# Kernel tuning notes

Measured on AMD Instinct MI355X. Metric: run time of the kernel, lower is better.

Reference implementation:

```python
import jax, jax.numpy as jnp
import numpy as np

N_TP = 4  # number of heterogeneous agent types (experts)


def _mlp(x, w1, b1, w2, b2, w3, b3):
    h = jax.nn.relu(x @ w1 + b1)
    h = jax.nn.relu(h @ w2 + b2)
    return h @ w3 + b3


def setup_inputs() -> dict:
    key = jax.random.key(0)
    ks = jax.random.split(key, 12)
    T, A, D, H, NA = 2048, 128, 64, 64, 16
    s = 0.05
    return {
        "obs": jax.random.normal(ks[0], (T, A, D), dtype=jnp.float32),
        "hete_pick": jax.random.randint(ks[1], (T, A), 0, N_TP, dtype=jnp.int64),
        "gp_sel_summary": jax.random.uniform(ks[2], (T, N_TP), dtype=jnp.float32),
        "W1": jax.random.normal(ks[3], (N_TP, D + N_TP, H), dtype=jnp.float32) * s,
        "b1": jnp.zeros((N_TP, H), jnp.float32),
        "W2": jax.random.normal(ks[4], (N_TP, H, H), dtype=jnp.float32) * s,
        "b2": jnp.zeros((N_TP, H), jnp.float32),
        "W3": jax.random.normal(ks[5], (N_TP, H, NA), dtype=jnp.float32) * s,
        "b3": jnp.zeros((N_TP, NA), jnp.float32),
        "cW1": jax.random.normal(ks[6], (D + N_TP, H), dtype=jnp.float32) * s,
        "cb1": jnp.zeros((H,), jnp.float32),
        "cW2": jax.random.normal(ks[7], (H, H), dtype=jnp.float32) * s,
        "cb2": jnp.zeros((H,), jnp.float32),
        "cW3": jax.random.normal(ks[8], (H, 1), dtype=jnp.float32) * s,
        "cb3": jnp.zeros((1,), jnp.float32),
    }


def reference(obs, hete_pick, gp_sel_summary, W1, b1, W2, b2, W3, b3,
              cW1, cb1, cW2, cb2, cW3, cb3):
    T, A, D = obs.shape
    n_tp = W1.shape[0]
    # hete_info_obs: broadcast group-selection summary over agents, concat to obs
    hete_info = jnp.broadcast_to(gp_sel_summary[:, None, :], (T, A, n_tp))
    x = jnp.concatenate([obs, hete_info.astype(obs.dtype)], axis=-1)  # [T,A,D+n_tp]
    xf = x.reshape(T * A, D + n_tp)
    tp = hete_pick.reshape(T * A)
    # per-type dispatch: mask -> sub-net -> scatter back (expressed as masked select)
    logits = jnp.zeros((T * A, W3.shape[-1]), obs.dtype)
    for t in range(n_tp):
        out_t = _mlp(xf, W1[t], b1[t], W2[t], b2[t], W3[t], b3[t])
        logits = jnp.where((tp == t)[:, None], out_t, logits)
    # central critic runs on all agents
    value = _mlp(xf, cW1, cb1, cW2, cb2, cW3, cb3)  # [T*A,1]
    out = jnp.concatenate([logits, value], axis=-1)  # [T*A, n_action+1]
    return out.reshape(T, A, -1)
```

## Files before the change

### kernel.cpp

```cpp
#include <hip/hip_runtime.h>
#include <stdint.h>


typedef float v4f __attribute__((ext_vector_type(4)));
typedef short v8s __attribute__((ext_vector_type(8)));

#define WP2_OFF 30720
#define WP3_OFF 51200

static __device__ __forceinline__ uint32_t rna_hi(float f) {
    union { float f; uint32_t u; } c; c.f = f;
    return (c.u + 0x8000u) >> 16;
}
static __device__ __forceinline__ uint32_t pk2(float a, float b) {
    union { float f; uint32_t u; } ca, cb; ca.f = a; cb.f = b;
    return ((ca.u + 0x8000u) >> 16) | ((cb.u + 0x8000u) & 0xffff0000u);
}

__global__ void prep_kernel(const float* __restrict__ W1, const float* __restrict__ cW1,
                            const float* __restrict__ b1, const float* __restrict__ cb1,
                            const float* __restrict__ W2, const float* __restrict__ cW2,
                            const float* __restrict__ W3, const float* __restrict__ cW3,
                            short* __restrict__ wp) {
    int b = blockIdx.x, lane = threadIdx.x;
    int nl = lane & 15, quad = lane >> 4;
    short frag[8];
    if (b < 60) {
        int e = b / 12, rem = b % 12, ks = rem / 4, nt = rem % 4;
        int n = nt * 16 + nl;
#pragma unroll
        for (int j = 0; j < 8; j++) {
            int k = ks * 32 + quad * 8 + j;
            float v = 0.f;
            if (k < 68)       v = (e < 4) ? W1[(e * 68 + k) * 64 + n] : cW1[k * 64 + n];
            else if (k == 68) v = (e < 4) ? b1[e * 64 + n] : cb1[n];
            frag[j] = (short)rna_hi(v);
        }
    } else if (b < 100) {
        int u = b - 60, e = u / 8, ks = (u % 8) / 4, nt = u % 4;
        int n = nt * 16 + nl;
#pragma unroll
        for (int j = 0; j < 8; j++) {
            int ka = (2 * ks + (j >> 2)) * 16 + quad * 4 + (j & 3);
            frag[j] = (short)rna_hi((e < 4) ? W2[(e * 64 + ka) * 64 + n] : cW2[ka * 64 + n]);
        }
    } else {
        int u = b - 100;
#pragma unroll
        for (int j = 0; j < 8; j++) {
            int ks = (u < 8) ? (u & 1) : (u - 8);
            int ka = (2 * ks + (j >> 2)) * 16 + quad * 4 + (j & 3);
            float v;
            if (u < 8) { int ee = u >> 1; v = W3[(ee * 64 + ka) * 16 + nl]; }
            else       { v = (nl == 0) ? cW3[ka] : 0.f; }
            frag[j] = (short)rna_hi(v);
        }
    }
    v8s pk = { frag[0], frag[1], frag[2], frag[3], frag[4], frag[5], frag[6], frag[7] };
    *(v8s*)(wp + (size_t)b * 512 + lane * 8) = pk;
}


__global__ __launch_bounds__(256) void main_kernel(
    const float* __restrict__ obs, const float* __restrict__ gp,
    const int* __restrict__ hete, const short* __restrict__ wp,
    const float* __restrict__ b2, const float* __restrict__ b3,
    const float* __restrict__ cb2, const float* __restrict__ cb3,
    float* __restrict__ out)
{
    int tid = threadIdx.x, wv = tid >> 6, lane = tid & 63;
    int ml = lane & 15, quad = lane >> 4;
    int base = (blockIdx.x * 4 + wv) * 32;

    v8s xf[2][2];
    v8s xg[2];
    int tpv[2];

#pragma unroll
    for (int tt = 0; tt < 2; tt++) {
        int tok = base + tt * 16 + ml;
        tpv[tt] = hete[tok];
        const float* xr = obs + (size_t)tok * 64 + quad * 8;
#pragma unroll
        for (int ks = 0; ks < 2; ks++) {
            float4 a = *(const float4*)(xr + ks * 32);
            float4 c = *(const float4*)(xr + ks * 32 + 4);
            union { uint32_t u[4]; v8s s; } cv;
            cv.u[0] = pk2(a.x, a.y); cv.u[1] = pk2(a.z, a.w);
            cv.u[2] = pk2(c.x, c.y); cv.u[3] = pk2(c.z, c.w);
            xf[ks][tt] = cv.s;
        }
        union { uint32_t u[4]; v8s s; } cg;
        if (quad == 0) {
            float4 g = *(const float4*)(gp + (size_t)(base >> 7) * 4);
            cg.u[0] = pk2(g.x, g.y); cg.u[1] = pk2(g.z, g.w);
            cg.u[2] = 0x00003F80u;
            cg.u[3] = 0;
        } else { cg.u[0] = 0; cg.u[1] = 0; cg.u[2] = 0; cg.u[3] = 0; }
        xg[tt] = cg.s;
    }

    float cb3v = cb3[0];
    float oL[2][4];
    float oV[2];
#pragma unroll
    for (int tt = 0; tt < 2; tt++) {
        oL[tt][0] = 0.f; oL[tt][1] = 0.f; oL[tt][2] = 0.f; oL[tt][3] = 0.f;
        oV[tt] = 0.f;
    }

    for (int ne = 0; ne < 5; ne++) {
        v4f acc[2][4];
#pragma unroll
        for (int tt = 0; tt < 2; tt++)
#pragma unroll
            for (int nt = 0; nt < 4; nt++) acc[tt][nt] = (v4f){0.f, 0.f, 0.f, 0.f};
#pragma unroll
        for (int ks = 0; ks < 3; ks++) {
            v8s wa[4];
#pragma unroll
            for (int nt = 0; nt < 4; nt++)
                wa[nt] = *(const v8s*)(wp + (size_t)((ne * 3 + ks) * 4 + nt) * 512 + lane * 8);
#pragma unroll
            for (int tt = 0; tt < 2; tt++) {
                v8s xb = (ks < 2) ? xf[ks][tt] : xg[tt];
#pragma unroll
                for (int nt = 0; nt < 4; nt++)
                    acc[tt][nt] = __builtin_amdgcn_mfma_f32_16x16x32_bf16(wa[nt], xb, acc[tt][nt], 0, 0, 0);
            }
        }
        v8s wa2[2][4];
#pragma unroll
        for (int ks2 = 0; ks2 < 2; ks2++)
#pragma unroll
            for (int nt = 0; nt < 4; nt++)
                wa2[ks2][nt] = *(const v8s*)(wp + WP2_OFF +
                    (size_t)((ne * 2 + ks2) * 4 + nt) * 512 + lane * 8);
        v8s w3f[2];
#pragma unroll
        for (int ks2 = 0; ks2 < 2; ks2++)
            w3f[ks2] = *(const v8s*)(wp + WP3_OFF +
                (size_t)((ne < 4) ? (ne * 2 + ks2) : (8 + ks2)) * 512 + lane * 8);
        const float* B2 = (ne < 4) ? (b2 + ne * 64) : cb2;

#pragma unroll
        for (int tt = 0; tt < 2; tt++) {
            v8s hf[2];
#pragma unroll
            for (int ks2 = 0; ks2 < 2; ks2++) {
                union { uint32_t u[4]; v8s s; } cv;
                cv.u[0] = pk2(fmaxf(acc[tt][2 * ks2][0], 0.f),     fmaxf(acc[tt][2 * ks2][1], 0.f));
                cv.u[1] = pk2(fmaxf(acc[tt][2 * ks2][2], 0.f),     fmaxf(acc[tt][2 * ks2][3], 0.f));
                cv.u[2] = pk2(fmaxf(acc[tt][2 * ks2 + 1][0], 0.f), fmaxf(acc[tt][2 * ks2 + 1][1], 0.f));
                cv.u[3] = pk2(fmaxf(acc[tt][2 * ks2 + 1][2], 0.f), fmaxf(acc[tt][2 * ks2 + 1][3], 0.f));
                hf[ks2] = cv.s;
            }
            v4f a2[4];
#pragma unroll
            for (int nt = 0; nt < 4; nt++)
                a2[nt] = *(const v4f*)(B2 + nt * 16 + quad * 4);
#pragma unroll
            for (int ks2 = 0; ks2 < 2; ks2++)
#pragma unroll
                for (int nt = 0; nt < 4; nt++)
                    a2[nt] = __builtin_amdgcn_mfma_f32_16x16x32_bf16(wa2[ks2][nt], hf[ks2], a2[nt], 0, 0, 0);
            v8s hf2[2];
#pragma unroll
            for (int ks2 = 0; ks2 < 2; ks2++) {
                union { uint32_t u[4]; v8s s; } cv;
                cv.u[0] = pk2(fmaxf(a2[2 * ks2][0], 0.f),     fmaxf(a2[2 * ks2][1], 0.f));
                cv.u[1] = pk2(fmaxf(a2[2 * ks2][2], 0.f),     fmaxf(a2[2 * ks2][3], 0.f));
                cv.u[2] = pk2(fmaxf(a2[2 * ks2 + 1][0], 0.f), fmaxf(a2[2 * ks2 + 1][1], 0.f));
                cv.u[3] = pk2(fmaxf(a2[2 * ks2 + 1][2], 0.f), fmaxf(a2[2 * ks2 + 1][3], 0.f));
                hf2[ks2] = cv.s;
            }
            v4f a3;
            if (ne < 4) a3 = *(const v4f*)(b3 + ne * 16 + quad * 4);
            else        a3 = (v4f){0.f, 0.f, 0.f, 0.f};
#pragma unroll
            for (int ks2 = 0; ks2 < 2; ks2++)
                a3 = __builtin_amdgcn_mfma_f32_16x16x32_bf16(w3f[ks2], hf2[ks2], a3, 0, 0, 0);

            if (ne < 4) {
#pragma unroll
                for (int rr = 0; rr < 4; rr++)
                    oL[tt][rr] = (tpv[tt] == ne) ? a3[rr] : oL[tt][rr];
            } else {
                oV[tt] = a3[0] + cb3v;
            }
        }
    }

#pragma unroll
    for (int tt = 0; tt < 2; tt++) {
        int tok = base + tt * 16 + ml;
        size_t o = (size_t)tok * 17 + quad * 4;
        out[o + 0] = oL[tt][0];
        out[o + 1] = oL[tt][1];
        out[o + 2] = oL[tt][2];
        out[o + 3] = oL[tt][3];
        if (quad == 0) out[(size_t)tok * 17 + 16] = oV[tt];
    }
}


extern "C" void kernel_launch(void* const* d_in, const int* in_sizes, int n_in,
                              void* d_out, int out_size, void* d_ws, size_t ws_size,
                              hipStream_t stream) {
    const float* obs = (const float*)d_in[0];
    const int*  hete = (const int*)d_in[1];
    const float* gp  = (const float*)d_in[2];
    const float* W1  = (const float*)d_in[3];
    const float* b1  = (const float*)d_in[4];
    const float* W2  = (const float*)d_in[5];
    const float* b2  = (const float*)d_in[6];
    const float* W3  = (const float*)d_in[7];
    const float* b3  = (const float*)d_in[8];
    const float* cW1 = (const float*)d_in[9];
    const float* cb1 = (const float*)d_in[10];
    const float* cW2 = (const float*)d_in[11];
    const float* cb2 = (const float*)d_in[12];
    const float* cW3 = (const float*)d_in[13];
    const float* cb3 = (const float*)d_in[14];
    float* out = (float*)d_out;

    short* wp = (short*)d_ws;

    prep_kernel<<<110,   64, 0, stream>>>(W1, cW1, b1, cb1, W2, cW2, W3, cW3, wp);
    main_kernel<<<2048, 256, 0, stream>>>(obs, gp, hete, wp,
                                          b2, b3, cb2, cb3, out);
}
```

Baseline: 160.8 us.

## Stage expert weights in double-buffered LDS and process 64 tokens per wave

Each block now copies one expert's packed bf16 weight fragments into a double-buffered shared-memory slot, prefetching the next expert into registers while the current one is computed. Each wave handles 64 tokens instead of 32, the grid is halved, and biases are hoisted out of the per-tile loop. The aim is to cut repeated global/L2 weight fetches per wave and amortise them over more tokens. The cost is extra registers for the prefetch, LDS use, barriers per expert, and fewer blocks in flight.

```diff
diff --git a/kernel.cpp b/kernel.cpp
--- a/kernel.cpp
+++ b/kernel.cpp
@@ -7,6 +7,7 @@
 
 #define WP2_OFF 30720
 #define WP3_OFF 51200
+#define NSLOT   1408
 
 static __device__ __forceinline__ uint32_t rna_hi(float f) {
     union { float f; uint32_t u; } c; c.f = f;
@@ -60,24 +61,37 @@
     *(v8s*)(wp + (size_t)b * 512 + lane * 8) = pk;
 }
 
-
-__global__ __launch_bounds__(256) void main_kernel(
+static __device__ __forceinline__ int src_of(int n, int k, int s) {
+    if (k < 3) return n * 768 + s;
+    if (k < 5) return 3840 + n * 512 + (s - 768);
+    return 6400 + n * 128 + (s - 1280);
+}
+
+
+__global__ __launch_bounds__(256, 2) void main_kernel(
     const float* __restrict__ obs, const float* __restrict__ gp,
     const int* __restrict__ hete, const short* __restrict__ wp,
     const float* __restrict__ b2, const float* __restrict__ b3,
     const float* __restrict__ cb2, const float* __restrict__ cb3,
     float* __restrict__ out)
 {
+    __shared__ __align__(16) uint4 buf[2][NSLOT];
     int tid = threadIdx.x, wv = tid >> 6, lane = tid & 63;
     int ml = lane & 15, quad = lane >> 4;
-    int base = (blockIdx.x * 4 + wv) * 32;
-
-    v8s xf[2][2];
-    v8s xg[2];
-    int tpv[2];
-
-#pragma unroll
-    for (int tt = 0; tt < 2; tt++) {
+    int base = blockIdx.x * 256 + wv * 64;
+    const uint4* w4 = (const uint4*)wp;
+
+#pragma unroll
+    for (int k = 0; k < 6; k++) {
+        int s = tid + k * 256;
+        if (k < 5 || tid < 128) buf[0][s] = w4[src_of(0, k, s)];
+    }
+
+    v8s xf[2][4];
+    v8s xg[4];
+    int tpv[4];
+#pragma unroll
+    for (int tt = 0; tt < 4; tt++) {
         int tok = base + tt * 16 + ml;
         tpv[tt] = hete[tok];
         const float* xr = obs + (size_t)tok * 64 + quad * 8;
@@ -101,64 +115,79 @@
     }
 
     float cb3v = cb3[0];
-    float oL[2][4];
-    float oV[2];
-#pragma unroll
-    for (int tt = 0; tt < 2; tt++) {
+    float oL[4][4], oV[4];
+#pragma unroll
+    for (int tt = 0; tt < 4; tt++) {
         oL[tt][0] = 0.f; oL[tt][1] = 0.f; oL[tt][2] = 0.f; oL[tt][3] = 0.f;
         oV[tt] = 0.f;
     }
 
+    __syncthreads();
+
+#pragma unroll 1
     for (int ne = 0; ne < 5; ne++) {
-        v4f acc[2][4];
-#pragma unroll
-        for (int tt = 0; tt < 2; tt++)
-#pragma unroll
-            for (int nt = 0; nt < 4; nt++) acc[tt][nt] = (v4f){0.f, 0.f, 0.f, 0.f};
-#pragma unroll
-        for (int ks = 0; ks < 3; ks++) {
-            v8s wa[4];
+        uint4 pf[6];
+        if (ne < 4) {
+#pragma unroll
+            for (int k = 0; k < 6; k++) {
+                int s = tid + k * 256;
+                if (k < 5 || tid < 128) pf[k] = w4[src_of(ne + 1, k, s)];
+            }
+        }
+
+        const short* cw = (const short*)&buf[ne & 1][0];
+
+        v8s wa[3][4];
+#pragma unroll
+        for (int ks = 0; ks < 3; ks++)
 #pragma unroll
             for (int nt = 0; nt < 4; nt++)
-                wa[nt] = *(const v8s*)(wp + (size_t)((ne * 3 + ks) * 4 + nt) * 512 + lane * 8);
-#pragma unroll
-            for (int tt = 0; tt < 2; tt++) {
+                wa[ks][nt] = *(const v8s*)(cw + (ks * 4 + nt) * 512 + lane * 8);
+        v8s wa2[2][4];
+#pragma unroll
+        for (int ks2 = 0; ks2 < 2; ks2++)
+#pragma unroll
+            for (int nt = 0; nt < 4; nt++)
+                wa2[ks2][nt] = *(const v8s*)(cw + 6144 + (ks2 * 4 + nt) * 512 + lane * 8);
+        v8s w3f[2];
+#pragma unroll
+        for (int ks2 = 0; ks2 < 2; ks2++)
+            w3f[ks2] = *(const v8s*)(cw + 10240 + ks2 * 512 + lane * 8);
+
+        const float* B2 = (ne < 4) ? (b2 + ne * 64) : cb2;
+        v4f bv2[4];
+#pragma unroll
+        for (int nt = 0; nt < 4; nt++)
+            bv2[nt] = *(const v4f*)(B2 + nt * 16 + quad * 4);
+        v4f b3f;
+        if (ne < 4) b3f = *(const v4f*)(b3 + ne * 16 + quad * 4);
+        else        b3f = (v4f){0.f, 0.f, 0.f, 0.f};
+
+#pragma unroll
+        for (int tt = 0; tt < 4; tt++) {
+            v4f acc[4];
+#pragma unroll
+            for (int nt = 0; nt < 4; nt++) acc[nt] = (v4f){0.f, 0.f, 0.f, 0.f};
+#pragma unroll
+            for (int ks = 0; ks < 3; ks++) {
                 v8s xb = (ks < 2) ? xf[ks][tt] : xg[tt];
 #pragma unroll
                 for (int nt = 0; nt < 4; nt++)
-                    acc[tt][nt] = __builtin_amdgcn_mfma_f32_16x16x32_bf16(wa[nt], xb, acc[tt][nt], 0, 0, 0);
-            }
-        }
-        v8s wa2[2][4];
-#pragma unroll
-        for (int ks2 = 0; ks2 < 2; ks2++)
-#pragma unroll
-            for (int nt = 0; nt < 4; nt++)
-                wa2[ks2][nt] = *(const v8s*)(wp + WP2_OFF +
-                    (size_t)((ne * 2 + ks2) * 4 + nt) * 512 + lane * 8);
-        v8s w3f[2];
-#pragma unroll
-        for (int ks2 = 0; ks2 < 2; ks2++)
-            w3f[ks2] = *(const v8s*)(wp + WP3_OFF +
-                (size_t)((ne < 4) ? (ne * 2 + ks2) : (8 + ks2)) * 512 + lane * 8);
-        const float* B2 = (ne < 4) ? (b2 + ne * 64) : cb2;
-
-#pragma unroll
-        for (int tt = 0; tt < 2; tt++) {
+                    acc[nt] = __builtin_amdgcn_mfma_f32_16x16x32_bf16(wa[ks][nt], xb, acc[nt], 0, 0, 0);
+            }
             v8s hf[2];
 #pragma unroll
             for (int ks2 = 0; ks2 < 2; ks2++) {
                 union { uint32_t u[4]; v8s s; } cv;
-                cv.u[0] = pk2(fmaxf(acc[tt][2 * ks2][0], 0.f),     fmaxf(acc[tt][2 * ks2][1], 0.f));
-                cv.u[1] = pk2(fmaxf(acc[tt][2 * ks2][2], 0.f),     fmaxf(acc[tt][2 * ks2][3], 0.f));
-                cv.u[2] = pk2(fmaxf(acc[tt][2 * ks2 + 1][0], 0.f), fmaxf(acc[tt][2 * ks2 + 1][1], 0.f));
-                cv.u[3] = pk2(fmaxf(acc[tt][2 * ks2 + 1][2], 0.f), fmaxf(acc[tt][2 * ks2 + 1][3], 0.f));
+                cv.u[0] = pk2(fmaxf(acc[2 * ks2][0], 0.f),     fmaxf(acc[2 * ks2][1], 0.f));
+                cv.u[1] = pk2(fmaxf(acc[2 * ks2][2], 0.f),     fmaxf(acc[2 * ks2][3], 0.f));
+                cv.u[2] = pk2(fmaxf(acc[2 * ks2 + 1][0], 0.f), fmaxf(acc[2 * ks2 + 1][1], 0.f));
+                cv.u[3] = pk2(fmaxf(acc[2 * ks2 + 1][2], 0.f), fmaxf(acc[2 * ks2 + 1][3], 0.f));
                 hf[ks2] = cv.s;
             }
             v4f a2[4];
 #pragma unroll
-            for (int nt = 0; nt < 4; nt++)
-                a2[nt] = *(const v4f*)(B2 + nt * 16 + quad * 4);
+            for (int nt = 0; nt < 4; nt++) a2[nt] = bv2[nt];
 #pragma unroll
             for (int ks2 = 0; ks2 < 2; ks2++)
 #pragma unroll
@@ -174,9 +203,7 @@
                 cv.u[3] = pk2(fmaxf(a2[2 * ks2 + 1][2], 0.f), fmaxf(a2[2 * ks2 + 1][3], 0.f));
                 hf2[ks2] = cv.s;
             }
-            v4f a3;
-            if (ne < 4) a3 = *(const v4f*)(b3 + ne * 16 + quad * 4);
-            else        a3 = (v4f){0.f, 0.f, 0.f, 0.f};
+            v4f a3 = b3f;
 #pragma unroll
             for (int ks2 = 0; ks2 < 2; ks2++)
                 a3 = __builtin_amdgcn_mfma_f32_16x16x32_bf16(w3f[ks2], hf2[ks2], a3, 0, 0, 0);
@@ -189,10 +216,19 @@
                 oV[tt] = a3[0] + cb3v;
             }
         }
-    }
-
-#pragma unroll
-    for (int tt = 0; tt < 2; tt++) {
+
+        if (ne < 4) {
+#pragma unroll
+            for (int k = 0; k < 6; k++) {
+                int s = tid + k * 256;
+                if (k < 5 || tid < 128) buf[(ne + 1) & 1][s] = pf[k];
+            }
+            __syncthreads();
+        }
+    }
+
+#pragma unroll
+    for (int tt = 0; tt < 4; tt++) {
         int tok = base + tt * 16 + ml;
         size_t o = (size_t)tok * 17 + quad * 4;
         out[o + 0] = oL[tt][0];
@@ -227,6 +263,6 @@
     short* wp = (short*)d_ws;
 
     prep_kernel<<<110,   64, 0, stream>>>(W1, cW1, b1, cb1, W2, cW2, W3, cW3, wp);
-    main_kernel<<<2048, 256, 0, stream>>>(obs, gp, hete, wp,
+    main_kernel<<<1024, 256, 0, stream>>>(obs, gp, hete, wp,
                                           b2, b3, cb2, cb3, out);
 }
```

Result: slower. 175.0 us (+8.8%).
